# Performance work log

Measured on AMD Instinct MI355X. Metric: run time of the kernel, lower is better.

## Reference

```python
import jax, jax.numpy as jnp
import numpy as np

K = 32  # neighbors per point (self.k)

def setup_inputs() -> dict:
    key = jax.random.key(0)
    k1, k2 = jax.random.split(key)
    B, N, C = 16, 4096, 64
    x = jax.random.normal(k1, (B, N, C), dtype=jnp.float32)
    idx = jax.random.randint(k2, (B, N, K), 0, N, dtype=jnp.int64)
    return {"x": x, "idx": idx}

def reference(x, idx):
    # pooled[b, n, :] = mean_k x[b, idx[b, n, k], :]
    # gather per-batch: xb[ib] -> [N, K, C]
    gathered = jax.vmap(lambda xb, ib: xb[ib])(x, idx)  # [B, N, K, C]
    return gathered.mean(axis=2)  # [B, N, C]
```

## Files before the change

### kernel.cpp

```cpp
#include <hip/hip_runtime.h>


#define BB 16
#define NN 4096
#define KK 32
#define CC 64

__global__ void detect_idx64_kernel(const int* __restrict__ w,
                                    int* __restrict__ flag) {
    int t = threadIdx.x;
    int v = w[2 * t + 1];
    unsigned long long nz = __ballot(v != 0);
    if (t == 0) *flag = (nz == 0ULL) ? 1 : 0;
}

__global__ __launch_bounds__(256)
void gapool_kernel(const float* __restrict__ x,
                   const int* __restrict__ idx32,
                   const int* __restrict__ flag,
                   float* __restrict__ out) {
    const int is64 = *flag;

    const int wave = (blockIdx.x * blockDim.x + threadIdx.x) >> 6;
    const int lane = threadIdx.x & 63;
    const int b = wave >> 12;
    const int n = wave & (NN - 1);
    const int ksub = lane >> 4;
    const int c4   = lane & 15;

    const int ibase = (b * NN + n) * KK;
    int jv = 0;
    if (lane < KK) {
        jv = is64 ? idx32[2 * (ibase + lane)] : idx32[ibase + lane];
    }

    const float4* xb = (const float4*)x + (size_t)b * NN * (CC / 4);

    float4 acc = make_float4(0.f, 0.f, 0.f, 0.f);
#pragma unroll
    for (int ko = 0; ko < KK / 4; ++ko) {
        const int k = ko * 4 + ksub;
        const int j = __shfl(jv, k, 64);
        const float4 v = xb[j * (CC / 4) + c4];
        acc.x += v.x; acc.y += v.y; acc.z += v.z; acc.w += v.w;
    }

#pragma unroll
    for (int off = 16; off <= 32; off <<= 1) {
        acc.x += __shfl_xor(acc.x, off, 64);
        acc.y += __shfl_xor(acc.y, off, 64);
        acc.z += __shfl_xor(acc.z, off, 64);
        acc.w += __shfl_xor(acc.w, off, 64);
    }

    if (ksub == 0) {
        const float s = 1.0f / KK;
        float4 r = make_float4(acc.x * s, acc.y * s, acc.z * s, acc.w * s);
        ((float4*)out)[(size_t)(b * NN + n) * (CC / 4) + c4] = r;
    }
}

extern "C" void kernel_launch(void* const* d_in, const int* in_sizes, int n_in,
                              void* d_out, int out_size, void* d_ws, size_t ws_size,
                              hipStream_t stream) {
    const float* x     = (const float*)d_in[0];
    const int*   idx32 = (const int*)d_in[1];
    float*       out   = (float*)d_out;
    int*         flag  = (int*)d_ws;

    detect_idx64_kernel<<<1, 64, 0, stream>>>(idx32, flag);

    const int total_waves = BB * NN;
    const int blocks = total_waves / 4;
    gapool_kernel<<<blocks, 256, 0, stream>>>(x, idx32, flag, out);
}
```

Baseline: 97.56 us.

## Map one block per point with scalar per-channel gather loads

Each point now gets its own 64-thread block in which every lane owns one channel and loops over all 32 neighbors. Each lane loads the indices itself (uniform, likely scalar loads) and does scalar float gathers instead of float4 loads. This removes the index shuffles and the cross-lane reduction. The cost is narrower memory transactions, a serial dependency chain across the 32 neighbors, and four times as many small blocks.

```diff
diff --git a/kernel.cpp b/kernel.cpp
--- a/kernel.cpp
+++ b/kernel.cpp
@@ -14,50 +14,36 @@
     if (t == 0) *flag = (nz == 0ULL) ? 1 : 0;
 }
 
-__global__ __launch_bounds__(256)
+__global__ __launch_bounds__(64)
 void gapool_kernel(const float* __restrict__ x,
                    const int* __restrict__ idx32,
                    const int* __restrict__ flag,
                    float* __restrict__ out) {
+    const int point = blockIdx.x;
+    const int b = point >> 12;
+    const int c = threadIdx.x;
     const int is64 = *flag;
 
-    const int wave = (blockIdx.x * blockDim.x + threadIdx.x) >> 6;
-    const int lane = threadIdx.x & 63;
-    const int b = wave >> 12;
-    const int n = wave & (NN - 1);
-    const int ksub = lane >> 4;
-    const int c4   = lane & 15;
+    const float* __restrict__ xb = x + (size_t)b * NN * CC;
 
-    const int ibase = (b * NN + n) * KK;
-    int jv = 0;
-    if (lane < KK) {
-        jv = is64 ? idx32[2 * (ibase + lane)] : idx32[ibase + lane];
+    float acc = 0.0f;
+    if (is64) {
+        const int* __restrict__ ip = idx32 + (size_t)point * KK * 2;
+#pragma unroll
+        for (int k = 0; k < KK; ++k) {
+            const int j = ip[2 * k];
+            acc += xb[(size_t)j * CC + c];
+        }
+    } else {
+        const int* __restrict__ ip = idx32 + (size_t)point * KK;
+#pragma unroll
+        for (int k = 0; k < KK; ++k) {
+            const int j = ip[k];
+            acc += xb[(size_t)j * CC + c];
+        }
     }
 
-    const float4* xb = (const float4*)x + (size_t)b * NN * (CC / 4);
-
-    float4 acc = make_float4(0.f, 0.f, 0.f, 0.f);
-#pragma unroll
-    for (int ko = 0; ko < KK / 4; ++ko) {
-        const int k = ko * 4 + ksub;
-        const int j = __shfl(jv, k, 64);
-        const float4 v = xb[j * (CC / 4) + c4];
-        acc.x += v.x; acc.y += v.y; acc.z += v.z; acc.w += v.w;
-    }
-
-#pragma unroll
-    for (int off = 16; off <= 32; off <<= 1) {
-        acc.x += __shfl_xor(acc.x, off, 64);
-        acc.y += __shfl_xor(acc.y, off, 64);
-        acc.z += __shfl_xor(acc.z, off, 64);
-        acc.w += __shfl_xor(acc.w, off, 64);
-    }
-
-    if (ksub == 0) {
-        const float s = 1.0f / KK;
-        float4 r = make_float4(acc.x * s, acc.y * s, acc.z * s, acc.w * s);
-        ((float4*)out)[(size_t)(b * NN + n) * (CC / 4) + c4] = r;
-    }
+    out[(size_t)point * CC + c] = acc * (1.0f / KK);
 }
 
 extern "C" void kernel_launch(void* const* d_in, const int* in_sizes, int n_in,
@@ -70,7 +56,5 @@
 
     detect_idx64_kernel<<<1, 64, 0, stream>>>(idx32, flag);
 
-    const int total_waves = BB * NN;
-    const int blocks = total_waves / 4;
-    gapool_kernel<<<blocks, 256, 0, stream>>>(x, idx32, flag, out);
+    gapool_kernel<<<BB * NN, 64, 0, stream>>>(x, idx32, flag, out);
 }
```

New measurement: 95.55 us. 1.02x faster.
